# Optimization experiments

Hardware: AMD Instinct MI355X
Metric: run time of the kernel (lower is better)

## Reference

```python
import jax, jax.numpy as jnp
import numpy as np

H = 8  # n_head

def rel_shift(x):
    # x: [B, H, S, 2S-1] -> [B, H, S, S]
    B, h, S, _ = x.shape
    x_padded = jnp.pad(x, ((0, 0), (0, 0), (0, 0), (1, 0)))  # [B,H,S,2S]
    x_padded = x_padded.reshape(B, h, 2 * S, S)
    x = x_padded[:, :, 1:, :].reshape(B, h, S, 2 * S - 1)
    return x[:, :, :, :S]

def setup_inputs() -> dict:
    key = jax.random.key(0)
    ks = jax.random.split(key, 16)
    B, S, D = 8, 1024, 512
    C = D // H
    inp = {
        "query": jax.random.normal(ks[0], (B, S, D), jnp.float32),
        "key": jax.random.normal(ks[1], (B, S, D), jnp.float32),
        "value": jax.random.normal(ks[2], (B, S, D), jnp.float32),
        "pos_emb": jax.random.normal(ks[3], (1, 2 * S - 1, D), jnp.float32),
        "mask": jnp.zeros((B, S), dtype=bool),
        "Wq": jax.random.normal(ks[4], (D, D), jnp.float32) / np.sqrt(D),
        "bq": jnp.zeros((D,), jnp.float32),
        "Wk": jax.random.normal(ks[5], (D, D), jnp.float32) / np.sqrt(D),
        "bk": jnp.zeros((D,), jnp.float32),
        "Wv": jax.random.normal(ks[6], (D, D), jnp.float32) / np.sqrt(D),
        "bv": jnp.zeros((D,), jnp.float32),
        "Wpos": jax.random.normal(ks[7], (D, D), jnp.float32) / np.sqrt(D),
        "Wout": jax.random.normal(ks[8], (D, D), jnp.float32) / np.sqrt(D),
        "bout": jnp.zeros((D,), jnp.float32),
        "u_bias": jax.random.normal(ks[9], (H, C), jnp.float32) / np.sqrt(C),
        "v_bias": jax.random.normal(ks[10], (H, C), jnp.float32) / np.sqrt(C),
    }
    return inp

def reference(query, key, value, pos_emb, mask, Wq, bq, Wk, bk, Wv, bv,
              Wpos, Wout, bout, u_bias, v_bias):
    B, S, D = query.shape
    C = D // H
    # qkv projections -> [B, H, S, C]
    q = (query @ Wq + bq).reshape(B, S, H, C).transpose(0, 2, 1, 3)
    k = (key @ Wk + bk).reshape(B, S, H, C).transpose(0, 2, 1, 3)
    v = (value @ Wv + bv).reshape(B, S, H, C).transpose(0, 2, 1, 3)
    # positional projection: pos_emb [1, 2S-1, D] -> p [H, 2S-1, C]
    P = pos_emb.shape[1]
    p = (pos_emb[0] @ Wpos).reshape(P, H, C).transpose(1, 0, 2)
    q_u = q + u_bias[:, None, :]
    q_v = q + v_bias[:, None, :]
    matrix_ac = jnp.einsum('bhsc,bhtc->bhst', q_u, k)           # [B,H,S,S]
    matrix_bd = jnp.einsum('bhsc,htc->bhst', q_v, p)            # [B,H,S,2S-1]
    matrix_bd = rel_shift(matrix_bd)                            # [B,H,S,S]
    scores = (matrix_ac + matrix_bd) / jnp.sqrt(jnp.float32(C))
    scores = jnp.where(mask[:, None, None, :], -jnp.inf, scores)
    p_attn = jax.nn.softmax(scores, axis=-1)
    x = jnp.einsum('bhst,bhtc->bhsc', p_attn, v)
    x = x.transpose(0, 2, 1, 3).reshape(B, S, D)
    return x @ Wout + bout
```

## Files before the change

### kernel.cpp

```cpp
#include <hip/hip_runtime.h>
#include <math.h>

typedef unsigned short ushort_t;
typedef __attribute__((ext_vector_type(8))) short short8;
typedef __attribute__((ext_vector_type(4))) float f32x4;

#define MFMA(a,b,c) __builtin_amdgcn_mfma_f32_16x16x32_bf16((a),(b),(c),0,0,0)

#define BB 8
#define SS 1024
#define DD 512
#define HH 8
#define CC 64
#define PP 2047

static __device__ __forceinline__ ushort_t f2bf(float f) {
    unsigned u = __float_as_uint(f);
    u += 0x7fffu + ((u >> 16) & 1u);
    return (ushort_t)(u >> 16);
}
static __device__ __forceinline__ unsigned pack2(float a, float b) {
    return (unsigned)f2bf(a) | ((unsigned)f2bf(b) << 16);
}

__global__ __launch_bounds__(256) void wtrans_kernel(
    const float* __restrict__ Wq, const float* __restrict__ Wk,
    const float* __restrict__ Wv, const float* __restrict__ Wp,
    const float* __restrict__ Wo, ushort_t* __restrict__ wt)
{
    __shared__ float T[64][65];
    const int bid = blockIdx.x, tid = threadIdx.x;
    const int wi   = bid >> 6;
    const int tile = bid & 63;
    const float* Wsrc = (wi == 0) ? Wq : (wi == 1) ? Wk : (wi == 2) ? Wv
                      : (wi == 3) ? Wp : Wo;
    ushort_t* Wdst = wt + (size_t)wi * 262144;
    const int tk0 = (tile >> 3) * 64, tn0 = (tile & 7) * 64;
    const int r = tid >> 2, c4 = (tid & 3) * 16;
    #pragma unroll
    for (int rep = 0; rep < 4; ++rep) {
        float4 f = *(const float4*)(Wsrc + (size_t)(tk0 + r) * 512 + tn0 + c4 + rep * 4);
        T[r][c4 + rep * 4 + 0] = f.x; T[r][c4 + rep * 4 + 1] = f.y;
        T[r][c4 + rep * 4 + 2] = f.z; T[r][c4 + rep * 4 + 3] = f.w;
    }
    __syncthreads();
    #pragma unroll
    for (int rep = 0; rep < 4; ++rep) {
        uint2 u;
        u.x = pack2(T[c4 + rep * 4 + 0][r], T[c4 + rep * 4 + 1][r]);
        u.y = pack2(T[c4 + rep * 4 + 2][r], T[c4 + rep * 4 + 3][r]);
        *(uint2*)(Wdst + (size_t)(tn0 + r) * 512 + tk0 + c4 + rep * 4) = u;
    }
}

__global__ __launch_bounds__(256) void qkvpos_kernel(
    const float* __restrict__ Xq, const float* __restrict__ Xk,
    const float* __restrict__ Xv, const float* __restrict__ Xp,
    const ushort_t* __restrict__ wt,
    const float* __restrict__ bq, const float* __restrict__ bk,
    const float* __restrict__ bv,
    const float* __restrict__ ub, const float* __restrict__ vbias,
    ushort_t* __restrict__ qu, ushort_t* __restrict__ qvo,
    ushort_t* __restrict__ kbuf, ushort_t* __restrict__ vtb,
    ushort_t* __restrict__ pbuf)
{
    __shared__ __align__(16) ushort_t smem[64 * 72 + 128 * 72];
    ushort_t (*Xs)[72] = (ushort_t(*)[72])smem;
    ushort_t (*Ws)[72] = (ushort_t(*)[72])(smem + 64 * 72);
    ushort_t (*Es)[136] = (ushort_t(*)[136])smem;
    ushort_t (*EsT)[72] = (ushort_t(*)[72])smem;

    const int tid = threadIdx.x;
    const int wave = tid >> 6, lane = tid & 63, quad = lane >> 4, l16 = lane & 15;
    const int bid = blockIdx.x;
    const int nt = (bid >> 3) & 3;
    const int mt = (bid & 7) + 8 * (bid >> 5);
    const int n0 = nt * 128;
    int mode, mtl;
    if (mt < 128)      { mode = 0; mtl = mt; }
    else if (mt < 256) { mode = 1; mtl = mt - 128; }
    else if (mt < 384) { mode = 2; mtl = mt - 256; }
    else               { mode = 3; mtl = mt - 384; }
    const int m0 = mtl * 64;
    const float* X = (mode == 0) ? Xq : (mode == 1) ? Xk : (mode == 2) ? Xv : Xp;
    const ushort_t* W = wt + (size_t)mode * 262144;

    f32x4 acc[4][2];
    #pragma unroll
    for (int i = 0; i < 4; ++i)
        #pragma unroll
        for (int j = 0; j < 2; ++j) acc[i][j] = (f32x4){0.f, 0.f, 0.f, 0.f};

    const int xr = tid >> 2, xc = (tid & 3) * 16;
    int xrow = m0 + xr;
    if (mode == 3 && xrow > PP - 1) xrow = PP - 1;
    const int wr0 = tid >> 2, wc0 = (tid & 3) * 16;
    const int wr1 = (tid + 256) >> 2, wc1 = wc0;

    {
        const float* xp = X + (size_t)xrow * 512 + xc;
        float4 f0 = *(const float4*)xp;
        float4 f1 = *(const float4*)(xp + 4);
        float4 f2 = *(const float4*)(xp + 8);
        float4 f3 = *(const float4*)(xp + 12);
        uint4 a, bpk;
        a.x = pack2(f0.x, f0.y); a.y = pack2(f0.z, f0.w);
        a.z = pack2(f1.x, f1.y); a.w = pack2(f1.z, f1.w);
        bpk.x = pack2(f2.x, f2.y); bpk.y = pack2(f2.z, f2.w);
        bpk.z = pack2(f3.x, f3.y); bpk.w = pack2(f3.z, f3.w);
        *(uint4*)&Xs[xr][xc] = a;
        *(uint4*)&Xs[xr][xc + 8] = bpk;
        const ushort_t* wp0 = W + (size_t)(n0 + wr0) * 512 + wc0;
        const ushort_t* wp1 = W + (size_t)(n0 + wr1) * 512 + wc1;
        *(uint4*)&Ws[wr0][wc0]     = *(const uint4*)wp0;
        *(uint4*)&Ws[wr0][wc0 + 8] = *(const uint4*)(wp0 + 8);
        *(uint4*)&Ws[wr1][wc1]     = *(const uint4*)wp1;
        *(uint4*)&Ws[wr1][wc1 + 8] = *(const uint4*)(wp1 + 8);
    }
    __syncthreads();

    for (int k0 = 0; k0 < 512; k0 += 64) {
        const bool more = (k0 + 64) < 512;
        uint4 xa, xb, wv0a, wv0b, wv1a, wv1b;
        if (more) {
            const float* xp = X + (size_t)xrow * 512 + k0 + 64 + xc;
            float4 f0 = *(const float4*)xp;
            float4 f1 = *(const float4*)(xp + 4);
            float4 f2 = *(const float4*)(xp + 8);
            float4 f3 = *(const float4*)(xp + 12);
            xa.x = pack2(f0.x, f0.y); xa.y = pack2(f0.z, f0.w);
            xa.z = pack2(f1.x, f1.y); xa.w = pack2(f1.z, f1.w);
            xb.x = pack2(f2.x, f2.y); xb.y = pack2(f2.z, f2.w);
            xb.z = pack2(f3.x, f3.y); xb.w = pack2(f3.z, f3.w);
            const ushort_t* wp0 = W + (size_t)(n0 + wr0) * 512 + k0 + 64 + wc0;
            const ushort_t* wp1 = W + (size_t)(n0 + wr1) * 512 + k0 + 64 + wc1;
            wv0a = *(const uint4*)wp0; wv0b = *(const uint4*)(wp0 + 8);
            wv1a = *(const uint4*)wp1; wv1b = *(const uint4*)(wp1 + 8);
        }
        #pragma unroll
        for (int kk = 0; kk < 2; ++kk) {
            short8 av[4], bv4[2];
            #pragma unroll
            for (int ms = 0; ms < 4; ++ms)
                av[ms] = *(const short8*)&Xs[ms * 16 + l16][kk * 32 + quad * 8];
            #pragma unroll
            for (int ns = 0; ns < 2; ++ns)
                bv4[ns] = *(const short8*)&Ws[wave * 32 + ns * 16 + l16][kk * 32 + quad * 8];
            #pragma unroll
            for (int ms = 0; ms < 4; ++ms)
                #pragma unroll
                for (int ns = 0; ns < 2; ++ns)
                    acc[ms][ns] = MFMA(av[ms], bv4[ns], acc[ms][ns]);
        }
        if (more) {
            __syncthreads();
            *(uint4*)&Xs[xr][xc]       = xa;
            *(uint4*)&Xs[xr][xc + 8]   = xb;
            *(uint4*)&Ws[wr0][wc0]     = wv0a;
            *(uint4*)&Ws[wr0][wc0 + 8] = wv0b;
            *(uint4*)&Ws[wr1][wc1]     = wv1a;
            *(uint4*)&Ws[wr1][wc1 + 8] = wv1b;
            __syncthreads();
        }
    }
    __syncthreads();

    float b1c[2], b2c[2], b3c[2];
    #pragma unroll
    for (int ns = 0; ns < 2; ++ns) {
        const int gcol = n0 + wave * 32 + ns * 16 + l16;
        if (mode == 0) { b1c[ns] = bq[gcol]; b2c[ns] = ub[gcol]; b3c[ns] = vbias[gcol]; }
        else if (mode == 1) { b1c[ns] = bk[gcol]; }
        else if (mode == 2) { b1c[ns] = bv[gcol]; }
        else b1c[ns] = 0.f;
    }

    const int npass = (mode == 0) ? 2 : 1;
    for (int pass = 0; pass < npass; ++pass) {
        #pragma unroll
        for (int ms = 0; ms < 4; ++ms)
        #pragma unroll
        for (int ns = 0; ns < 2; ++ns)
        #pragma unroll
        for (int r = 0; r < 4; ++r) {
            const int lrow = ms * 16 + quad * 4 + r;
            const int lcol = wave * 32 + ns * 16 + l16;
            float v = acc[ms][ns][r];
            if (mode == 0) v += b1c[ns] + (pass == 0 ? b2c[ns] : b3c[ns]);
            else if (mode != 3) v += b1c[ns];
            if (mode == 2) EsT[lcol][lrow] = f2bf(v);
            else           Es[lrow][lcol]  = f2bf(v);
        }
        __syncthreads();
        if (mode == 2) {
            const int b = m0 >> 10;
            #pragma unroll
            for (int i = 0; i < 4; ++i) {
                int u = tid + 256 * i;
                int cl = u >> 3, off8 = (u & 7) * 8;
                uint4 d = *(const uint4*)&EsT[cl][off8];
                const int gcol = n0 + cl;
                ushort_t* dst = vtb + (((size_t)(b * HH + (gcol >> 6))) * CC + (gcol & 63)) * SS
                                + (m0 & 1023) + off8;
                *(uint4*)dst = d;
            }
        } else {
            #pragma unroll
            for (int i = 0; i < 4; ++i) {
                int u = tid + 256 * i;
                int seg = u >> 3, off8 = (u & 7) * 8;
                int sl = seg >> 1, hsel = seg & 1;
                int lc = hsel * 64 + off8;
                uint4 d = *(const uint4*)&Es[sl][lc];
                const int grow = m0 + sl;
                const int gcol = n0 + lc;
                if (mode == 3) {
                    if (grow < PP) {
                        ushort_t* dst = pbuf + ((size_t)(gcol >> 6) * PP + grow) * CC + (gcol & 63);
                        *(uint4*)dst = d;
                    }
                } else {
                    size_t idx = (((size_t)(grow >> 10) * HH + (gcol >> 6)) * SS + (grow & 1023)) * CC + (gcol & 63);
                    ushort_t* dst = (mode == 1) ? (kbuf + idx)
                                  : (pass == 0 ? (qu + idx) : (qvo + idx));
                    *(uint4*)dst = d;
                }
            }
        }
        if (pass + 1 < npass) __syncthreads();
    }
}

__global__ __launch_bounds__(256) void outproj_kernel(
    const ushort_t* __restrict__ X, const ushort_t* __restrict__ W,
    const float* __restrict__ b1, float* __restrict__ Yf)
{
    __shared__ __align__(16) ushort_t smem[64 * 72 + 128 * 72];
    ushort_t (*Xs)[72] = (ushort_t(*)[72])smem;
    ushort_t (*Ws)[72] = (ushort_t(*)[72])(smem + 64 * 72);

    const int tid = threadIdx.x;
    const int wave = tid >> 6, lane = tid & 63, quad = lane >> 4, l16 = lane & 15;
    const int bid = blockIdx.x;
    const int nt = (bid >> 3) & 3;
    const int mtl = (bid & 7) + 8 * (bid >> 5);
    const int n0 = nt * 128, m0 = mtl * 64;

    f32x4 acc[4][2];
    #pragma unroll
    for (int i = 0; i < 4; ++i)
        #pragma unroll
        for (int j = 0; j < 2; ++j) acc[i][j] = (f32x4){0.f, 0.f, 0.f, 0.f};

    const int xr = tid >> 2, xc = (tid & 3) * 16;
    const int wr0 = tid >> 2, wc0 = (tid & 3) * 16;
    const int wr1 = (tid + 256) >> 2, wc1 = wc0;

    {
        const ushort_t* xp = X + (size_t)(m0 + xr) * 512 + xc;
        *(uint4*)&Xs[xr][xc]     = *(const uint4*)xp;
        *(uint4*)&Xs[xr][xc + 8] = *(const uint4*)(xp + 8);
        const ushort_t* wp0 = W + (size_t)(n0 + wr0) * 512 + wc0;
        const ushort_t* wp1 = W + (size_t)(n0 + wr1) * 512 + wc1;
        *(uint4*)&Ws[wr0][wc0]     = *(const uint4*)wp0;
        *(uint4*)&Ws[wr0][wc0 + 8] = *(const uint4*)(wp0 + 8);
        *(uint4*)&Ws[wr1][wc1]     = *(const uint4*)wp1;
        *(uint4*)&Ws[wr1][wc1 + 8] = *(const uint4*)(wp1 + 8);
    }
    __syncthreads();

    for (int k0 = 0; k0 < 512; k0 += 64) {
        const bool more = (k0 + 64) < 512;
        uint4 xa, xb, wv0a, wv0b, wv1a, wv1b;
        if (more) {
            const ushort_t* xp = X + (size_t)(m0 + xr) * 512 + k0 + 64 + xc;
            xa = *(const uint4*)xp;
            xb = *(const uint4*)(xp + 8);
            const ushort_t* wp0 = W + (size_t)(n0 + wr0) * 512 + k0 + 64 + wc0;
            const ushort_t* wp1 = W + (size_t)(n0 + wr1) * 512 + k0 + 64 + wc1;
            wv0a = *(const uint4*)wp0; wv0b = *(const uint4*)(wp0 + 8);
            wv1a = *(const uint4*)wp1; wv1b = *(const uint4*)(wp1 + 8);
        }
        #pragma unroll
        for (int kk = 0; kk < 2; ++kk) {
            short8 av[4], bv4[2];
            #pragma unroll
            for (int ms = 0; ms < 4; ++ms)
                av[ms] = *(const short8*)&Xs[ms * 16 + l16][kk * 32 + quad * 8];
            #pragma unroll
            for (int ns = 0; ns < 2; ++ns)
                bv4[ns] = *(const short8*)&Ws[wave * 32 + ns * 16 + l16][kk * 32 + quad * 8];
            #pragma unroll
            for (int ms = 0; ms < 4; ++ms)
                #pragma unroll
                for (int ns = 0; ns < 2; ++ns)
                    acc[ms][ns] = MFMA(av[ms], bv4[ns], acc[ms][ns]);
        }
        if (more) {
            __syncthreads();
            *(uint4*)&Xs[xr][xc]       = xa;
            *(uint4*)&Xs[xr][xc + 8]   = xb;
            *(uint4*)&Ws[wr0][wc0]     = wv0a;
            *(uint4*)&Ws[wr0][wc0 + 8] = wv0b;
            *(uint4*)&Ws[wr1][wc1]     = wv1a;
            *(uint4*)&Ws[wr1][wc1 + 8] = wv1b;
            __syncthreads();
        }
    }

    #pragma unroll
    for (int ms = 0; ms < 4; ++ms)
    #pragma unroll
    for (int ns = 0; ns < 2; ++ns)
    #pragma unroll
    for (int r = 0; r < 4; ++r) {
        const int row = m0 + ms * 16 + quad * 4 + r;
        const int col = n0 + wave * 32 + ns * 16 + l16;
        Yf[(size_t)row * 512 + col] = acc[ms][ns][r] + b1[col];
    }
}

__global__ __launch_bounds__(512) void attn_kernel(
    const ushort_t* __restrict__ qu_g, const ushort_t* __restrict__ qv_g,
    const ushort_t* __restrict__ kb, const ushort_t* __restrict__ vt_g,
    const ushort_t* __restrict__ pbf, const unsigned char* __restrict__ mask,
    ushort_t* __restrict__ xg)
{
    const int bh = blockIdx.x;
    const int s0 = blockIdx.y * 128;
    const int b = bh >> 3, h = bh & 7;
    const int tid = threadIdx.x;
    const int wave = tid >> 6, lane = tid & 63, quad = lane >> 4, l16 = lane & 15;

    __shared__ __align__(16) ushort_t Ks[64][72];
    __shared__ __align__(16) ushort_t Vts[64][72];
    __shared__ __align__(16) ushort_t Pb[256][72];
    __shared__ __align__(16) ushort_t Pscr[8][16][72];

    const size_t qoff = ((size_t)bh * SS + s0 + wave * 16 + l16) * CC;
    short8 quA[2], qvA[2];
    quA[0] = *(const short8*)(qu_g + qoff + quad * 8);
    quA[1] = *(const short8*)(qu_g + qoff + 32 + quad * 8);
    qvA[0] = *(const short8*)(qv_g + qoff + quad * 8);
    qvA[1] = *(const short8*)(qv_g + qoff + 32 + quad * 8);

    f32x4 O[4];
    #pragma unroll
    for (int i = 0; i < 4; ++i) O[i] = (f32x4){0.f, 0.f, 0.f, 0.f};
    float lsum[4] = {0.f, 0.f, 0.f, 0.f};

    const ushort_t* kbase  = kb   + ((size_t)bh << 10) * CC;
    const ushort_t* vtbase = vt_g + ((size_t)bh << 6) * SS;
    const ushort_t* pbase  = pbf  + (size_t)h * PP * CC;
    const unsigned char* mbase = mask + b * SS;

    const int R0base = 896 - s0;
    const int uwread = 1008 - s0 - wave * 16;

    {
        const int r = tid >> 3, cc = (tid & 7) * 8;
        *(uint4*)&Ks[r][cc]  = *(const uint4*)(kbase + (size_t)r * CC + cc);
        *(uint4*)&Vts[r][cc] = *(const uint4*)(vtbase + (size_t)r * SS + cc);
        #pragma unroll
        for (int i = 0; i < 3; ++i) {
            int u = tid + 512 * i; int rr = u >> 3; int c2 = (u & 7) * 8;
            int gr = R0base + rr;
            int g = gr; if (g < 0) g = 0; if (g > PP - 1) g = PP - 1;
            *(uint4*)&Pb[gr & 255][c2] = *(const uint4*)(pbase + (size_t)g * CC + c2);
        }
    }
    __syncthreads();

    for (int t0 = 0; t0 < SS; t0 += 64) {
        const bool more = (t0 + 64) < SS;
        uint4 kp, vp, pp;
        const int r = tid >> 3, cc = (tid & 7) * 8;
        if (more) {
            kp = *(const uint4*)(kbase + (size_t)(t0 + 64 + r) * CC + cc);
            vp = *(const uint4*)(vtbase + (size_t)r * SS + t0 + 64 + cc);
            int g = R0base + t0 + 192 + r;
            if (g > PP - 1) g = PP - 1;
            pp = *(const uint4*)(pbase + (size_t)g * CC + cc);
        }

        f32x4 ac[4];
        #pragma unroll
        for (int ns = 0; ns < 4; ++ns) {
            ac[ns] = (f32x4){0.f, 0.f, 0.f, 0.f};
            #pragma unroll
            for (int kk = 0; kk < 2; ++kk) {
                short8 kf = *(const short8*)&Ks[ns * 16 + l16][kk * 32 + quad * 8];
                ac[ns] = MFMA(quA[kk], kf, ac[ns]);
            }
        }
        f32x4 bd[5];
        #pragma unroll
        for (int us = 0; us < 5; ++us) {
            bd[us] = (f32x4){0.f, 0.f, 0.f, 0.f};
            #pragma unroll
            for (int kk = 0; kk < 2; ++kk) {
                short8 pf = *(const short8*)&Pb[(uwread + t0 + us * 16 + l16) & 255][kk * 32 + quad * 8];
                bd[us] = MFMA(qvA[kk], pf, bd[us]);
            }
        }

        bool mk[4];
        #pragma unroll
        for (int ns = 0; ns < 4; ++ns) mk[ns] = mbase[t0 + ns * 16 + l16] != 0;

        float pvv[4][4];
        #pragma unroll
        for (int rr = 0; rr < 4; ++rr) {
            const int sl = quad * 4 + rr;
            const int d = l16 + 15 - sl;
            const int srcl = quad * 16 + (d & 15);
            const bool use_hi = d >= 16;
            #pragma unroll
            for (int ns = 0; ns < 4; ++ns) {
                float lo = __shfl(bd[ns][rr], srcl, 64);
                float hi = __shfl(bd[ns + 1][rr], srcl, 64);
                float bdv = use_hi ? hi : lo;
                float p = __expf((ac[ns][rr] + bdv) * 0.125f - 40.f);
                p = mk[ns] ? 0.f : p;
                pvv[ns][rr] = p;
                lsum[rr] += p;
            }
        }

        #pragma unroll
        for (int ns = 0; ns < 4; ++ns)
            #pragma unroll
            for (int rr = 0; rr < 4; ++rr)
                Pscr[wave][quad * 4 + rr][ns * 16 + l16] = f2bf(pvv[ns][rr]);
        short8 pA0 = *(const short8*)&Pscr[wave][l16][quad * 8];
        short8 pA1 = *(const short8*)&Pscr[wave][l16][32 + quad * 8];

        #pragma unroll
        for (int ns = 0; ns < 4; ++ns) {
            short8 v0 = *(const short8*)&Vts[ns * 16 + l16][quad * 8];
            short8 v1 = *(const short8*)&Vts[ns * 16 + l16][32 + quad * 8];
            O[ns] = MFMA(pA0, v0, O[ns]);
            O[ns] = MFMA(pA1, v1, O[ns]);
        }

        if (more) {
            __syncthreads();
            *(uint4*)&Ks[r][cc]  = kp;
            *(uint4*)&Vts[r][cc] = vp;
            *(uint4*)&Pb[(R0base + t0 + 192 + r) & 255][cc] = pp;
            __syncthreads();
        }
    }

    #pragma unroll
    for (int rr = 0; rr < 4; ++rr) {
        float s = lsum[rr];
        s += __shfl_xor(s, 1, 64); s += __shfl_xor(s, 2, 64);
        s += __shfl_xor(s, 4, 64); s += __shfl_xor(s, 8, 64);
        const float inv = 1.0f / s;
        #pragma unroll
        for (int ns = 0; ns < 4; ++ns)
            Pscr[wave][quad * 4 + rr][ns * 16 + l16] = f2bf(O[ns][rr] * inv);
    }
    {
        const ushort_t* src = &Pscr[wave][lane >> 2][(lane & 3) * 16];
        uint4 u0 = *(const uint4*)src;
        uint4 u1 = *(const uint4*)(src + 8);
        const int srow = s0 + wave * 16 + (lane >> 2);
        ushort_t* dst = xg + ((size_t)b * SS + srow) * DD + h * CC + (lane & 3) * 16;
        *(uint4*)dst = u0;
        *(uint4*)(dst + 8) = u1;
    }
}

extern "C" void kernel_launch(void* const* d_in, const int* in_sizes, int n_in,
                              void* d_out, int out_size, void* d_ws, size_t ws_size,
                              hipStream_t stream)
{
    (void)in_sizes; (void)n_in; (void)out_size; (void)ws_size;

    const float* query = (const float*)d_in[0];
    const float* key_  = (const float*)d_in[1];
    const float* value = (const float*)d_in[2];
    const float* pos   = (const float*)d_in[3];
    const unsigned char* mask = (const unsigned char*)d_in[4];
    const float* Wq   = (const float*)d_in[5];
    const float* bq   = (const float*)d_in[6];
    const float* Wk   = (const float*)d_in[7];
    const float* bk   = (const float*)d_in[8];
    const float* Wv   = (const float*)d_in[9];
    const float* bv   = (const float*)d_in[10];
    const float* Wpos = (const float*)d_in[11];
    const float* Wout = (const float*)d_in[12];
    const float* bout = (const float*)d_in[13];
    const float* ub   = (const float*)d_in[14];
    const float* vb   = (const float*)d_in[15];

    const size_t NBS = (size_t)BB * SS * DD;
    const size_t NP  = (size_t)PP * DD;
    const size_t NW  = (size_t)DD * DD;

    ushort_t* wt   = (ushort_t*)d_ws;
    ushort_t* qu   = wt + 5 * NW;
    ushort_t* qv   = qu + NBS;
    ushort_t* kbuf = qv + NBS;
    ushort_t* vtb  = kbuf + NBS;
    ushort_t* pbuf = vtb + NBS;
    ushort_t* xg   = pbuf + NP;

    ushort_t* WtO = wt + 4 * NW;

    wtrans_kernel<<<dim3(320), dim3(256), 0, stream>>>(Wq, Wk, Wv, Wpos, Wout, wt);

    qkvpos_kernel<<<dim3(1664), dim3(256), 0, stream>>>(
        query, key_, value, pos, wt, bq, bk, bv, ub, vb,
        qu, qv, kbuf, vtb, pbuf);

    attn_kernel<<<dim3(64, 8), dim3(512), 0, stream>>>(qu, qv, kbuf, vtb, pbuf, mask, xg);

    outproj_kernel<<<dim3(512), dim3(256), 0, stream>>>(xg, WtO, bout, (float*)d_out);
}
```

Measured before the change: 225.9 us.

## Drop LDS staging in attention, load K/V/P fragments directly and double rows per wave

The attention kernel no longer stages K, V^T and positional rows through shared memory with double-buffered prefetch and block barriers. Each wave now reads its MFMA fragments straight from global memory (relying on caches) and handles 32 query rows instead of 16, so the fragments are reused across two row tiles. The 16-row offset between the two tiles lets one set of shared positional fragments serve both tiles' rel-shift windows. The block shrinks to 256 threads and s_setprio raises priority around the PV MFMAs. The aim is to remove barrier stalls and LDS traffic, at the cost of more register pressure and uncoalesced global and L2 loads.

```diff
diff --git a/kernel.cpp b/kernel.cpp
--- a/kernel.cpp
+++ b/kernel.cpp
@@ -320,7 +320,7 @@
     }
 }
 
-__global__ __launch_bounds__(512) void attn_kernel(
+__global__ __launch_bounds__(256) void attn_kernel(
     const ushort_t* __restrict__ qu_g, const ushort_t* __restrict__ qv_g,
     const ushort_t* __restrict__ kb, const ushort_t* __restrict__ vt_g,
     const ushort_t* __restrict__ pbf, const unsigned char* __restrict__ mask,
@@ -332,141 +332,123 @@
     const int tid = threadIdx.x;
     const int wave = tid >> 6, lane = tid & 63, quad = lane >> 4, l16 = lane & 15;
 
-    __shared__ __align__(16) ushort_t Ks[64][72];
-    __shared__ __align__(16) ushort_t Vts[64][72];
-    __shared__ __align__(16) ushort_t Pb[256][72];
-    __shared__ __align__(16) ushort_t Pscr[8][16][72];
-
-    const size_t qoff = ((size_t)bh * SS + s0 + wave * 16 + l16) * CC;
-    short8 quA[2], qvA[2];
-    quA[0] = *(const short8*)(qu_g + qoff + quad * 8);
-    quA[1] = *(const short8*)(qu_g + qoff + 32 + quad * 8);
-    qvA[0] = *(const short8*)(qv_g + qoff + quad * 8);
-    qvA[1] = *(const short8*)(qv_g + qoff + 32 + quad * 8);
-
-    f32x4 O[4];
-    #pragma unroll
-    for (int i = 0; i < 4; ++i) O[i] = (f32x4){0.f, 0.f, 0.f, 0.f};
-    float lsum[4] = {0.f, 0.f, 0.f, 0.f};
+    __shared__ __align__(16) ushort_t Pscr[4][16][72];
+
+    const int r0 = s0 + wave * 32;
+
+    short8 quA[2][2], qvA[2][2];
+    #pragma unroll
+    for (int m = 0; m < 2; ++m) {
+        const size_t qoff = ((size_t)bh * SS + r0 + m * 16 + l16) * CC;
+        quA[m][0] = *(const short8*)(qu_g + qoff + quad * 8);
+        quA[m][1] = *(const short8*)(qu_g + qoff + 32 + quad * 8);
+        qvA[m][0] = *(const short8*)(qv_g + qoff + quad * 8);
+        qvA[m][1] = *(const short8*)(qv_g + qoff + 32 + quad * 8);
+    }
+
+    f32x4 O[2][4];
+    float lsum[2][4];
+    #pragma unroll
+    for (int m = 0; m < 2; ++m)
+        #pragma unroll
+        for (int i = 0; i < 4; ++i) {
+            O[m][i] = (f32x4){0.f, 0.f, 0.f, 0.f};
+            lsum[m][i] = 0.f;
+        }
 
     const ushort_t* kbase  = kb   + ((size_t)bh << 10) * CC;
     const ushort_t* vtbase = vt_g + ((size_t)bh << 6) * SS;
     const ushort_t* pbase  = pbf  + (size_t)h * PP * CC;
     const unsigned char* mbase = mask + b * SS;
 
-    const int R0base = 896 - s0;
-    const int uwread = 1008 - s0 - wave * 16;
-
-    {
-        const int r = tid >> 3, cc = (tid & 7) * 8;
-        *(uint4*)&Ks[r][cc]  = *(const uint4*)(kbase + (size_t)r * CC + cc);
-        *(uint4*)&Vts[r][cc] = *(const uint4*)(vtbase + (size_t)r * SS + cc);
-        #pragma unroll
-        for (int i = 0; i < 3; ++i) {
-            int u = tid + 512 * i; int rr = u >> 3; int c2 = (u & 7) * 8;
-            int gr = R0base + rr;
-            int g = gr; if (g < 0) g = 0; if (g > PP - 1) g = PP - 1;
-            *(uint4*)&Pb[gr & 255][c2] = *(const uint4*)(pbase + (size_t)g * CC + c2);
-        }
-    }
-    __syncthreads();
+    const int jb0 = 992 - s0 - wave * 32;
 
     for (int t0 = 0; t0 < SS; t0 += 64) {
-        const bool more = (t0 + 64) < SS;
-        uint4 kp, vp, pp;
-        const int r = tid >> 3, cc = (tid & 7) * 8;
-        if (more) {
-            kp = *(const uint4*)(kbase + (size_t)(t0 + 64 + r) * CC + cc);
-            vp = *(const uint4*)(vtbase + (size_t)r * SS + t0 + 64 + cc);
-            int g = R0base + t0 + 192 + r;
-            if (g > PP - 1) g = PP - 1;
-            pp = *(const uint4*)(pbase + (size_t)g * CC + cc);
-        }
-
-        f32x4 ac[4];
+        const f32x4 z = (f32x4){0.f, 0.f, 0.f, 0.f};
+
+        f32x4 ac[2][4];
         #pragma unroll
         for (int ns = 0; ns < 4; ++ns) {
-            ac[ns] = (f32x4){0.f, 0.f, 0.f, 0.f};
-            #pragma unroll
-            for (int kk = 0; kk < 2; ++kk) {
-                short8 kf = *(const short8*)&Ks[ns * 16 + l16][kk * 32 + quad * 8];
-                ac[ns] = MFMA(quA[kk], kf, ac[ns]);
+            const ushort_t* kp = kbase + (size_t)(t0 + ns * 16 + l16) * CC;
+            short8 k0 = *(const short8*)(kp + quad * 8);
+            short8 k1 = *(const short8*)(kp + 32 + quad * 8);
+            ac[0][ns] = MFMA(quA[0][1], k1, MFMA(quA[0][0], k0, z));
+            ac[1][ns] = MFMA(quA[1][1], k1, MFMA(quA[1][0], k0, z));
+        }
+
+        f32x4 bd[2][5];
+        #pragma unroll
+        for (int j = 0; j < 6; ++j) {
+            int g = jb0 + t0 + j * 16 + l16;
+            g = (g > PP - 1) ? (PP - 1) : g;
+            const ushort_t* pp_ = pbase + (size_t)g * CC;
+            short8 p0 = *(const short8*)(pp_ + quad * 8);
+            short8 p1 = *(const short8*)(pp_ + 32 + quad * 8);
+            if (j < 5)  bd[1][j]     = MFMA(qvA[1][1], p1, MFMA(qvA[1][0], p0, z));
+            if (j >= 1) bd[0][j - 1] = MFMA(qvA[0][1], p1, MFMA(qvA[0][0], p0, z));
+        }
+
+        short8 vf0[4], vf1[4];
+        #pragma unroll
+        for (int ns = 0; ns < 4; ++ns) {
+            const ushort_t* vp = vtbase + (size_t)(ns * 16 + l16) * SS + t0;
+            vf0[ns] = *(const short8*)(vp + quad * 8);
+            vf1[ns] = *(const short8*)(vp + 32 + quad * 8);
+        }
+
+        bool mk[4];
+        #pragma unroll
+        for (int ns = 0; ns < 4; ++ns) mk[ns] = mbase[t0 + ns * 16 + l16] != 0;
+
+        #pragma unroll
+        for (int m = 0; m < 2; ++m) {
+            #pragma unroll
+            for (int rr = 0; rr < 4; ++rr) {
+                const int sl = quad * 4 + rr;
+                const int d = l16 + 15 - sl;
+                const int srcl = quad * 16 + (d & 15);
+                const bool hi = d >= 16;
+                float sh[5];
+                #pragma unroll
+                for (int us = 0; us < 5; ++us)
+                    sh[us] = __shfl(bd[m][us][rr], srcl, 64);
+                #pragma unroll
+                for (int ns = 0; ns < 4; ++ns) {
+                    float bdv = hi ? sh[ns + 1] : sh[ns];
+                    float p = __expf((ac[m][ns][rr] + bdv) * 0.125f - 40.f);
+                    p = mk[ns] ? 0.f : p;
+                    lsum[m][rr] += p;
+                    Pscr[wave][quad * 4 + rr][ns * 16 + l16] = f2bf(p);
+                }
             }
-        }
-        f32x4 bd[5];
-        #pragma unroll
-        for (int us = 0; us < 5; ++us) {
-            bd[us] = (f32x4){0.f, 0.f, 0.f, 0.f};
-            #pragma unroll
-            for (int kk = 0; kk < 2; ++kk) {
-                short8 pf = *(const short8*)&Pb[(uwread + t0 + us * 16 + l16) & 255][kk * 32 + quad * 8];
-                bd[us] = MFMA(qvA[kk], pf, bd[us]);
+            short8 pA0 = *(const short8*)&Pscr[wave][l16][quad * 8];
+            short8 pA1 = *(const short8*)&Pscr[wave][l16][32 + quad * 8];
+            __builtin_amdgcn_s_setprio(1);
+            #pragma unroll
+            for (int ns = 0; ns < 4; ++ns) {
+                O[m][ns] = MFMA(pA0, vf0[ns], O[m][ns]);
+                O[m][ns] = MFMA(pA1, vf1[ns], O[m][ns]);
             }
-        }
-
-        bool mk[4];
-        #pragma unroll
-        for (int ns = 0; ns < 4; ++ns) mk[ns] = mbase[t0 + ns * 16 + l16] != 0;
-
-        float pvv[4][4];
+            __builtin_amdgcn_s_setprio(0);
+        }
+    }
+
+    #pragma unroll
+    for (int m = 0; m < 2; ++m) {
         #pragma unroll
         for (int rr = 0; rr < 4; ++rr) {
-            const int sl = quad * 4 + rr;
-            const int d = l16 + 15 - sl;
-            const int srcl = quad * 16 + (d & 15);
-            const bool use_hi = d >= 16;
-            #pragma unroll
-            for (int ns = 0; ns < 4; ++ns) {
-                float lo = __shfl(bd[ns][rr], srcl, 64);
-                float hi = __shfl(bd[ns + 1][rr], srcl, 64);
-                float bdv = use_hi ? hi : lo;
-                float p = __expf((ac[ns][rr] + bdv) * 0.125f - 40.f);
-                p = mk[ns] ? 0.f : p;
-                pvv[ns][rr] = p;
-                lsum[rr] += p;
-            }
-        }
-
-        #pragma unroll
-        for (int ns = 0; ns < 4; ++ns)
-            #pragma unroll
-            for (int rr = 0; rr < 4; ++rr)
-                Pscr[wave][quad * 4 + rr][ns * 16 + l16] = f2bf(pvv[ns][rr]);
-        short8 pA0 = *(const short8*)&Pscr[wave][l16][quad * 8];
-        short8 pA1 = *(const short8*)&Pscr[wave][l16][32 + quad * 8];
-
-        #pragma unroll
-        for (int ns = 0; ns < 4; ++ns) {
-            short8 v0 = *(const short8*)&Vts[ns * 16 + l16][quad * 8];
-            short8 v1 = *(const short8*)&Vts[ns * 16 + l16][32 + quad * 8];
-            O[ns] = MFMA(pA0, v0, O[ns]);
-            O[ns] = MFMA(pA1, v1, O[ns]);
-        }
-
-        if (more) {
-            __syncthreads();
-            *(uint4*)&Ks[r][cc]  = kp;
-            *(uint4*)&Vts[r][cc] = vp;
-            *(uint4*)&Pb[(R0base + t0 + 192 + r) & 255][cc] = pp;
-            __syncthreads();
-        }
-    }
-
-    #pragma unroll
-    for (int rr = 0; rr < 4; ++rr) {
-        float s = lsum[rr];
-        s += __shfl_xor(s, 1, 64); s += __shfl_xor(s, 2, 64);
-        s += __shfl_xor(s, 4, 64); s += __shfl_xor(s, 8, 64);
-        const float inv = 1.0f / s;
-        #pragma unroll
-        for (int ns = 0; ns < 4; ++ns)
-            Pscr[wave][quad * 4 + rr][ns * 16 + l16] = f2bf(O[ns][rr] * inv);
-    }
-    {
+            float s = lsum[m][rr];
+            s += __shfl_xor(s, 1, 64); s += __shfl_xor(s, 2, 64);
+            s += __shfl_xor(s, 4, 64); s += __shfl_xor(s, 8, 64);
+            const float inv = 1.0f / s;
+            #pragma unroll
+            for (int ns = 0; ns < 4; ++ns)
+                Pscr[wave][quad * 4 + rr][ns * 16 + l16] = f2bf(O[m][ns][rr] * inv);
+        }
         const ushort_t* src = &Pscr[wave][lane >> 2][(lane & 3) * 16];
         uint4 u0 = *(const uint4*)src;
         uint4 u1 = *(const uint4*)(src + 8);
-        const int srow = s0 + wave * 16 + (lane >> 2);
+        const int srow = r0 + m * 16 + (lane >> 2);
         ushort_t* dst = xg + ((size_t)b * SS + srow) * DD + h * CC + (lane & 3) * 16;
         *(uint4*)dst = u0;
         *(uint4*)(dst + 8) = u1;
@@ -516,7 +498,7 @@
         query, key_, value, pos, wt, bq, bk, bv, ub, vb,
         qu, qv, kbuf, vtb, pbuf);
 
-    attn_kernel<<<dim3(64, 8), dim3(512), 0, stream>>>(qu, qv, kbuf, vtb, pbuf, mask, xg);
+    attn_kernel<<<dim3(64, 8), dim3(256), 0, stream>>>(qu, qv, kbuf, vtb, pbuf, mask, xg);
 
     outproj_kernel<<<dim3(512), dim3(256), 0, stream>>>(xg, WtO, bout, (float*)d_out);
 }
```

Result: slower. 307.1 us (+35.9%).
